# Kernel optimization log

Hardware: AMD Instinct MI355X
Metric: run time of the kernel (lower is better)

Reference implementation:

```python
import jax, jax.numpy as jnp
import numpy as np

N, IN_DIM, E_RAW, N_GRAPHS, HEADS = 50000, 128, 800000, 256, 2
NEG_ATT, NEG_ACT, EPS = 0.2, 0.01, 1e-5


def _gat(x, src, dst, W, a_src, a_dst, bias):
    # PyG GATConv: x' = xW per head; alpha = softmax_over_dst(leaky_relu(a_s.h_src + a_d.h_dst, 0.2))
    H, C = a_src.shape
    n = x.shape[0]
    h = (x @ W).reshape(n, H, C)                                  # [N,H,C]
    al_s = jnp.einsum('nhc,hc->nh', h, a_src)                     # [N,H]
    al_d = jnp.einsum('nhc,hc->nh', h, a_dst)                     # [N,H]
    e = jax.nn.leaky_relu(al_s[src] + al_d[dst], NEG_ATT)         # [E,H]
    m = jax.ops.segment_max(e, dst, num_segments=n)               # per-dst max (stable softmax)
    ee = jnp.exp(e - m[dst])
    s = jax.ops.segment_sum(ee, dst, num_segments=n)
    alpha = ee / (s[dst] + 1e-16)                                 # [E,H]
    out = jax.ops.segment_sum(h[src] * alpha[:, :, None], dst, num_segments=n)
    return out.reshape(n, H * C) + bias


def _bn(x, g, b):
    # training-mode BatchNorm1d over nodes (biased variance), eps=1e-5
    m = jnp.mean(x, 0)
    v = jnp.var(x, 0)
    return (x - m) * jax.lax.rsqrt(v + EPS) * g + b


def setup_inputs() -> dict:
    key = jax.random.key(0)
    ks = jax.random.split(key, 20)
    H, C1, C2, C3 = HEADS, 32, 64, 128
    rn = lambda i, sh, s=0.05: jax.random.normal(ks[i], sh, jnp.float32) * s
    inp = dict(
        x=jax.random.normal(ks[0], (N, IN_DIM), jnp.float32),
        edge_index=jax.random.randint(ks[1], (2, E_RAW), 0, N, jnp.int32),
        edge_weigth=jax.random.uniform(ks[2], (E_RAW,), jnp.float32),
        batch=jnp.sort(jax.random.randint(ks[3], (N,), 0, N_GRAPHS, jnp.int32)),
        W1=rn(4, (IN_DIM, H * C1)), a_src1=rn(5, (H, C1)), a_dst1=rn(6, (H, C1)),
        b1=jnp.zeros((H * C1,), jnp.float32), g1=jnp.ones((H * C1,), jnp.float32), be1=jnp.zeros((H * C1,), jnp.float32),
        W2=rn(7, (H * C1, H * C2)), a_src2=rn(8, (H, C2)), a_dst2=rn(9, (H, C2)),
        b2=jnp.zeros((H * C2,), jnp.float32), g2=jnp.ones((H * C2,), jnp.float32), be2=jnp.zeros((H * C2,), jnp.float32),
        W3=rn(10, (H * C2, H * C3)), a_src3=rn(11, (H, C3)), a_dst3=rn(12, (H, C3)),
        b3=jnp.zeros((H * C3,), jnp.float32), g3=jnp.ones((H * C3,), jnp.float32), be3=jnp.zeros((H * C3,), jnp.float32),
        Wc1=rn(13, (H * C1 + H * C2 + H * C3, 128)), bc1=jnp.zeros((128,), jnp.float32),
        Wc2=rn(14, (128, 64)), bc2=jnp.zeros((64,), jnp.float32),
        Wc3=rn(15, (64, 2)), bc3=jnp.zeros((2,), jnp.float32),
    )
    return inp


def reference(x, edge_index, edge_weigth, batch,
              W1, a_src1, a_dst1, b1, g1, be1,
              W2, a_src2, a_dst2, b2, g2, be2,
              W3, a_src3, a_dst3, b3, g3, be3,
              Wc1, bc1, Wc2, bc2, Wc3, bc3):
    n = x.shape[0]
    loops = jnp.arange(n, dtype=edge_index.dtype)  # GATConv add_self_loops=True
    src = jnp.concatenate([edge_index[0], loops])
    dst = jnp.concatenate([edge_index[1], loops])
    lr = lambda t: jax.nn.leaky_relu(t, NEG_ACT)
    x1 = lr(_bn(_gat(x, src, dst, W1, a_src1, a_dst1, b1), g1, be1))
    x2 = lr(_bn(_gat(x1, src, dst, W2, a_src2, a_dst2, b2), g2, be2))
    x3 = lr(_bn(_gat(x2, src, dst, W3, a_src3, a_dst3, b3), g3, be3))
    p = jnp.concatenate([
        jax.ops.segment_sum(x1, batch, num_segments=N_GRAPHS),
        jax.ops.segment_sum(x2, batch, num_segments=N_GRAPHS),
        jax.ops.segment_sum(x3, batch, num_segments=N_GRAPHS)], axis=1)
    h = lr(p @ Wc1 + bc1)
    h = lr(h @ Wc2 + bc2)
    return h @ Wc3 + bc3
```

## Files before the change

### kernel.cpp

```cpp
#include <hip/hip_runtime.h>
#include <hip/hip_fp16.h>
#include <math.h>

#define N_NODES 50000
#define E_RAW_N 800000
#define E_TOT   (E_RAW_N + N_NODES)
#define NGRAPH  256
#define POOL_F  448
#define SCAN_B  196
#define NSLICE  4
#define MBLK    391
#define EBLK    3321
#define PBLK    391

using f16x8 = __attribute__((ext_vector_type(8))) _Float16;
using f32x4 = __attribute__((ext_vector_type(4))) float;


template<int K, int F>
__device__ void do_wt(const float* __restrict__ W, __half* __restrict__ WT, int blk) {
    int i = blk * 256 + threadIdx.x;
    if (i >= F * (K / 8)) return;
    int f = i / (K / 8);
    int kb = (i % (K / 8)) * 8;
    __half tmp[8];
#pragma unroll
    for (int j = 0; j < 8; ++j) tmp[j] = __float2half(W[(size_t)(kb + j) * F + f]);
    *reinterpret_cast<uint4*>(WT + (size_t)f * K + kb) = *reinterpret_cast<uint4*>(tmp);
}


__global__ void k_init(int* __restrict__ deg, float* __restrict__ p,
                       float* __restrict__ bn,
                       const float* __restrict__ W1, const float* __restrict__ W2,
                       const float* __restrict__ W3, __half* __restrict__ WT1,
                       __half* __restrict__ WT2, __half* __restrict__ WT3) {
    int b = blockIdx.x;
    if (b < 448) {
        int i = b * 256 + threadIdx.x;
        if (i < N_NODES) deg[i] = 0;
        if (i < NGRAPH * POOL_F) p[i] = 0.f;
        if (i < NSLICE * 512 * 3) bn[i] = 0.f;
    } else {
        int wb = b - 448;
        if (wb < 4)       do_wt<128, 64>(W1, WT1, wb);
        else if (wb < 8)  do_wt<64, 128>(W2, WT2, wb - 4);
        else              do_wt<128, 256>(W3, WT3, wb - 8);
    }
}


__device__ inline void degrank_body(int bid, const int* __restrict__ dst_raw,
                                    int* __restrict__ deg, int* __restrict__ rank) {
    int e = bid * 256 + threadIdx.x;
    if (e >= E_TOT) return;
    int d = (e < E_RAW_N) ? dst_raw[e] : (e - E_RAW_N);
    rank[e] = atomicAdd(&deg[d], 1);
}

__global__ void k_scan1(const int* __restrict__ deg, int* __restrict__ bsum) {
    __shared__ int red[256];
    int i = blockIdx.x * 256 + threadIdx.x;
    int v = (i < N_NODES) ? deg[i] : 0;
    red[threadIdx.x] = v;
    __syncthreads();
    for (int o = 128; o > 0; o >>= 1) {
        if (threadIdx.x < o) red[threadIdx.x] += red[threadIdx.x + o];
        __syncthreads();
    }
    if (threadIdx.x == 0) bsum[blockIdx.x] = red[0];
}

__global__ void k_scan3(const int* __restrict__ deg, const int* __restrict__ bsum,
                        int* __restrict__ rowstart) {
    __shared__ int pre[256];
    __shared__ int s[256];
    int tid = threadIdx.x;
    pre[tid] = (tid < (int)blockIdx.x) ? bsum[tid] : 0;
    int i = blockIdx.x * 256 + tid;
    int v = (i < N_NODES) ? deg[i] : 0;
    s[tid] = v;
    __syncthreads();
    for (int o = 128; o > 0; o >>= 1) {
        if (tid < o) pre[tid] += pre[tid + o];
        __syncthreads();
    }
    for (int o = 1; o < 256; o <<= 1) {
        int t = (tid >= o) ? s[tid - o] : 0;
        __syncthreads();
        s[tid] += t;
        __syncthreads();
    }
    if (i < N_NODES) rowstart[i] = pre[0] + s[tid] - v;
    if (i == 0) rowstart[N_NODES] = E_TOT;
}

__global__ void k_fill(const int* __restrict__ ei, const int* __restrict__ rowstart,
                       const int* __restrict__ rank, int* __restrict__ adj) {
    int e = blockIdx.x * blockDim.x + threadIdx.x;
    if (e >= E_TOT) return;
    int s, d;
    if (e < E_RAW_N) { s = ei[e]; d = ei[E_RAW_N + e]; }
    else             { s = d = e - E_RAW_N; }
    adj[rowstart[d] + rank[e]] = s;
}


template<int F>
__device__ void bnpool_body(int bid, const __half* __restrict__ x,
                            const float* __restrict__ bnP, const float* __restrict__ g,
                            const float* __restrict__ be, const int* __restrict__ batch,
                            float* __restrict__ p, int poff) {
    constexpr int F2 = F / 2;
    constexpr int NGRP = 512 / F;
    constexpr int NPB = 128;
    int f2 = threadIdx.x % F2;
    int grp = threadIdx.x / F2;
    int f = 2 * f2;
    const float invN = 1.f / (float)N_NODES;
    float sm0 = 0.f, sm1 = 0.f, sq0 = 0.f, sq1 = 0.f;
#pragma unroll
    for (int s = 0; s < NSLICE; ++s) {
        sm0 += bnP[s * 2 * F + f];     sm1 += bnP[s * 2 * F + f + 1];
        sq0 += bnP[s * 2 * F + F + f]; sq1 += bnP[s * 2 * F + F + f + 1];
    }
    float m0 = sm0 * invN, m1 = sm1 * invN;
    float v0 = sq0 * invN - m0 * m0;
    float v1 = sq1 * invN - m1 * m1;
    float sc0 = rsqrtf(v0 + 1e-5f) * g[f];
    float sc1 = rsqrtf(v1 + 1e-5f) * g[f + 1];
    float bb0 = be[f] - m0 * sc0;
    float bb1 = be[f + 1] - m1 * sc1;
    int n0 = bid * NPB;
    int nend = n0 + NPB; if (nend > N_NODES) nend = N_NODES;
    int n = n0 + grp;
    if (n >= nend) return;
    float p0 = 0.f, p1 = 0.f;
    int cg = batch[n];
    for (; n < nend; n += NGRP) {
        float2 xv = __half22float2(*reinterpret_cast<const __half2*>(x + (size_t)n * F + f));
        float y0 = xv.x * sc0 + bb0; y0 = y0 > 0.f ? y0 : 0.01f * y0;
        float y1 = xv.y * sc1 + bb1; y1 = y1 > 0.f ? y1 : 0.01f * y1;
        int bg = batch[n];
        if (bg != cg) {
            atomicAdd(&p[cg * POOL_F + poff + f], p0);
            atomicAdd(&p[cg * POOL_F + poff + f + 1], p1);
            p0 = p1 = 0.f; cg = bg;
        }
        p0 += y0; p1 += y1;
    }
    atomicAdd(&p[cg * POOL_F + poff + f], p0);
    atomicAdd(&p[cg * POOL_F + poff + f + 1], p1);
}

template<int F>
__global__ void k_bnpool(const __half* __restrict__ x, const float* __restrict__ bnP,
                         const float* __restrict__ g, const float* __restrict__ be,
                         const int* __restrict__ batch, float* __restrict__ p, int poff) {
    bnpool_body<F>(blockIdx.x, x, bnP, g, be, batch, p, poff);
}


template<int K, int F, bool BNIN, typename TIN, typename TOUT, int SIDE>
__global__ void __launch_bounds__(256) k_mfma(
        const TIN* __restrict__ x, const __half* __restrict__ WT,
        const float* __restrict__ bnP,
        const float* __restrict__ g, const float* __restrict__ be,
        const float* __restrict__ a_src, const float* __restrict__ a_dst,
        void* __restrict__ hout, float* __restrict__ al_s, float* __restrict__ al_d,
        const int* __restrict__ dst_raw, int* __restrict__ deg, int* __restrict__ rank,
        const int* __restrict__ batch, float* __restrict__ pp, int poff) {
    if constexpr (SIDE == 1) {
        if (blockIdx.x >= MBLK) { degrank_body(blockIdx.x - MBLK, dst_raw, deg, rank); return; }
    } else if constexpr (SIDE == 2) {
        if (blockIdx.x >= MBLK) {
            bnpool_body<K>(blockIdx.x - MBLK, (const __half*)x, bnP, g, be, batch, pp, poff);
            return;
        }
    }
    constexpr int NF = F / 16;
    constexpr int KS = K / 32;
    constexpr int MT = 2;
    __shared__ float scs[K], bbs[K];
    int tid = threadIdx.x;
    if constexpr (BNIN) {
        const float invN = 1.f / (float)N_NODES;
        for (int i = tid; i < K; i += 256) {
            float sm = 0.f, sq = 0.f;
#pragma unroll
            for (int s = 0; s < NSLICE; ++s) {
                sm += bnP[s * 2 * K + i];
                sq += bnP[s * 2 * K + K + i];
            }
            float mean = sm * invN;
            float var  = sq * invN - mean * mean;
            float sc = rsqrtf(var + 1e-5f) * g[i];
            scs[i] = sc;
            bbs[i] = be[i] - mean * sc;
        }
        __syncthreads();
    }
    int wave = tid >> 6, lane = tid & 63;
    int col = lane & 15;
    int kg  = lane >> 4;
    long n_base = ((long)blockIdx.x * 4 + wave) * (MT * 16);
    if (n_base >= N_NODES) return;

    bool mv[MT];
#pragma unroll
    for (int m = 0; m < MT; ++m) mv[m] = (n_base + m * 16) < N_NODES;

    f32x4 acc[MT][NF];
#pragma unroll
    for (int m = 0; m < MT; ++m)
#pragma unroll
        for (int t = 0; t < NF; ++t) acc[m][t] = (f32x4){0.f, 0.f, 0.f, 0.f};

    for (int ks = 0; ks < KS; ++ks) {
        int kb = ks * 32 + kg * 8;
        f16x8 af[MT];
#pragma unroll
        for (int m = 0; m < MT; ++m) {
            if (!mv[m]) { af[m] = (f16x8){}; continue; }
            long nrow = n_base + m * 16 + col;
            if constexpr (sizeof(TIN) == 2) {
                uint4 u = *reinterpret_cast<const uint4*>((const __half*)x + nrow * K + kb);
                if constexpr (BNIN) {
                    const __half* hp = reinterpret_cast<const __half*>(&u);
                    f16x8 a;
#pragma unroll
                    for (int j = 0; j < 8; ++j) {
                        float y = __half2float(hp[j]) * scs[kb + j] + bbs[kb + j];
                        y = y > 0.f ? y : 0.01f * y;
                        a[j] = (_Float16)y;
                    }
                    af[m] = a;
                } else {
                    af[m] = *reinterpret_cast<const f16x8*>(&u);
                }
            } else {
                const float* xp = (const float*)x + nrow * K + kb;
                float4 v0 = *reinterpret_cast<const float4*>(xp);
                float4 v1 = *reinterpret_cast<const float4*>(xp + 4);
                f16x8 a;
                a[0] = (_Float16)v0.x; a[1] = (_Float16)v0.y;
                a[2] = (_Float16)v0.z; a[3] = (_Float16)v0.w;
                a[4] = (_Float16)v1.x; a[5] = (_Float16)v1.y;
                a[6] = (_Float16)v1.z; a[7] = (_Float16)v1.w;
                af[m] = a;
            }
        }
#pragma unroll
        for (int t = 0; t < NF; ++t) {
            f16x8 bf = *reinterpret_cast<const f16x8*>(WT + (size_t)(t * 16 + col) * K + kb);
            acc[0][t] = __builtin_amdgcn_mfma_f32_16x16x32_f16(af[0], bf, acc[0][t], 0, 0, 0);
            if constexpr (MT > 1)
                acc[1][t] = __builtin_amdgcn_mfma_f32_16x16x32_f16(af[1], bf, acc[1][t], 0, 0, 0);
        }
    }

#pragma unroll
    for (int m = 0; m < MT; ++m) {
        if (!mv[m]) continue;
#pragma unroll
        for (int t = 0; t < NF; ++t) {
#pragma unroll
            for (int r = 0; r < 4; ++r) {
                long n = n_base + m * 16 + kg * 4 + r;
                float v = acc[m][t][r];
                if constexpr (sizeof(TOUT) == 1) {
                    int pk = __builtin_amdgcn_cvt_pk_fp8_f32(v, v, 0, false);
                    reinterpret_cast<unsigned char*>(hout)[n * F + t * 16 + col] =
                        (unsigned char)(pk & 0xff);
                } else {
                    reinterpret_cast<__half*>(hout)[n * F + t * 16 + col] = __float2half(v);
                }
            }
        }
#pragma unroll
        for (int r = 0; r < 4; ++r) {
            float ss0 = 0.f, sd0 = 0.f, ss1 = 0.f, sd1 = 0.f;
#pragma unroll
            for (int t = 0; t < NF; ++t) {
                float v = acc[m][t][r];
                float as = a_src[t * 16 + col];
                float ad = a_dst[t * 16 + col];
                if (t < NF / 2) { ss0 += v * as; sd0 += v * ad; }
                else            { ss1 += v * as; sd1 += v * ad; }
            }
#pragma unroll
            for (int o = 1; o < 16; o <<= 1) {
                ss0 += __shfl_xor(ss0, o); sd0 += __shfl_xor(sd0, o);
                ss1 += __shfl_xor(ss1, o); sd1 += __shfl_xor(sd1, o);
            }
            if (col == 0) {
                long n = n_base + m * 16 + kg * 4 + r;
                al_s[n * 2]     = ss0; al_s[n * 2 + 1] = ss1;
                al_d[n * 2]     = sd0; al_d[n * 2 + 1] = sd1;
            }
        }
    }
}


template<bool FP8> struct PayT;
template<> struct PayT<false> { using T = uint4; };
template<> struct PayT<true>  { using T = uint2; };

template<bool FP8>
__device__ inline void accum8(typename PayT<FP8>::T u, float ee, float acc[8]) {
    if constexpr (FP8) {
        auto f0 = __builtin_amdgcn_cvt_pk_f32_fp8(u.x, false);
        auto f1 = __builtin_amdgcn_cvt_pk_f32_fp8(u.x, true);
        auto f2 = __builtin_amdgcn_cvt_pk_f32_fp8(u.y, false);
        auto f3 = __builtin_amdgcn_cvt_pk_f32_fp8(u.y, true);
        acc[0] += ee * f0[0]; acc[1] += ee * f0[1];
        acc[2] += ee * f1[0]; acc[3] += ee * f1[1];
        acc[4] += ee * f2[0]; acc[5] += ee * f2[1];
        acc[6] += ee * f3[0]; acc[7] += ee * f3[1];
    } else {
        float2 f0 = __half22float2(*reinterpret_cast<const __half2*>(&u.x));
        float2 f1 = __half22float2(*reinterpret_cast<const __half2*>(&u.y));
        float2 f2 = __half22float2(*reinterpret_cast<const __half2*>(&u.z));
        float2 f3 = __half22float2(*reinterpret_cast<const __half2*>(&u.w));
        acc[0] += ee * f0.x; acc[1] += ee * f0.y;
        acc[2] += ee * f1.x; acc[3] += ee * f1.y;
        acc[4] += ee * f2.x; acc[5] += ee * f2.y;
        acc[6] += ee * f3.x; acc[7] += ee * f3.y;
    }
}

template<int F, int C, bool FP8>
__global__ void __launch_bounds__(256) k_gather(
        const int* __restrict__ rowstart, const int* __restrict__ adj,
        const void* __restrict__ hv, const float* __restrict__ al_s,
        const float* __restrict__ al_d, const float* __restrict__ bias,
        __half* __restrict__ xpre) {
    using LT = typename PayT<FP8>::T;
    constexpr int HPL = 8;
    constexpr int LPE = F / HPL;
    constexpr int EPI = 64 / LPE;
    constexpr int UNR = (EPI >= 8) ? 4 : (16 / EPI);
    constexpr int STEP = UNR * EPI;
    constexpr unsigned RSH = FP8 ? 8 : ((F == 64) ? 7 : 8);
    int wave = (blockIdx.x * 256 + threadIdx.x) >> 6;
    int lane = threadIdx.x & 63;
    if (wave >= N_NODES) return;
    int n = wave;
    int rs = rowstart[n], re = rowstart[n + 1];
    float2 aldv = *reinterpret_cast<const float2*>(al_d + n * 2);

    const int es = lane / LPE;
    const int fl = lane % LPE;
    const unsigned fi = fl * HPL;
    const int hd = (fi >= C) ? 1 : 0;
    const float alh = hd ? aldv.y : aldv.x;
    const char* base = (const char*)hv;
    const char* alsb = (const char*)al_s;
    const unsigned fioff = FP8 ? fi : fi * 2;

    float acc[HPL];
#pragma unroll
    for (int j = 0; j < HPL; ++j) acc[j] = 0.f;
    float seh = 0.f;

    int nsteps = (re - rs + STEP - 1) / STEP;
    unsigned sN[UNR];
#pragma unroll
    for (int u = 0; u < UNR; ++u) {
        int e = rs + u * EPI + es;
        sN[u] = (unsigned)adj[min(e, re - 1)];
    }
    for (int t = 0; t < nsteps; ++t) {
        int ibase = rs + t * STEP;
        unsigned sC[UNR];
#pragma unroll
        for (int u = 0; u < UNR; ++u) sC[u] = sN[u];
        if (t + 1 < nsteps) {
            int nb = ibase + STEP;
#pragma unroll
            for (int u = 0; u < UNR; ++u) {
                int e = nb + u * EPI + es;
                sN[u] = (unsigned)adj[min(e, re - 1)];
            }
        }
        float alsN[UNR];
        LT hvN[UNR];
#pragma unroll
        for (int u = 0; u < UNR; ++u) {
            alsN[u] = *reinterpret_cast<const float*>(alsb + ((sC[u] << 3) | (unsigned)(hd << 2)));
            hvN[u] = *reinterpret_cast<const LT*>(base + ((sC[u] << RSH) + fioff));
        }
#pragma unroll
        for (int u = 0; u < UNR; ++u) {
            bool valid = (ibase + u * EPI + es) < re;
            float v = alsN[u] + alh; v = v > 0.f ? v : 0.2f * v;
            v = fminf(v, 80.f);
            float ee = valid ? __expf(v) : 0.f;
            seh += ee;
            accum8<FP8>(hvN[u], ee, acc);
        }
    }

#pragma unroll
    for (int o = LPE; o < 64; o <<= 1) {
        seh += __shfl_xor(seh, o);
#pragma unroll
        for (int j = 0; j < HPL; ++j) acc[j] += __shfl_xor(acc[j], o);
    }

    if (es == 0) {
        float inv = 1.f / (seh + 1e-16f);
        const float* bp = bias + fi;
        __half2 o0 = __floats2half2_rn(acc[0] * inv + bp[0], acc[1] * inv + bp[1]);
        __half2 o1 = __floats2half2_rn(acc[2] * inv + bp[2], acc[3] * inv + bp[3]);
        __half2 o2 = __floats2half2_rn(acc[4] * inv + bp[4], acc[5] * inv + bp[5]);
        __half2 o3 = __floats2half2_rn(acc[6] * inv + bp[6], acc[7] * inv + bp[7]);
        uint4 u;
        u.x = *reinterpret_cast<unsigned int*>(&o0);
        u.y = *reinterpret_cast<unsigned int*>(&o1);
        u.z = *reinterpret_cast<unsigned int*>(&o2);
        u.w = *reinterpret_cast<unsigned int*>(&o3);
        *reinterpret_cast<uint4*>(xpre + (size_t)n * F + fi) = u;
    }
}


template<int F>
__global__ void __launch_bounds__(256) k_bnstats(const __half* __restrict__ x,
        float* __restrict__ bnP) {
    constexpr int SLOTS = F / 8;
    constexpr int RPI   = 256 / SLOTS;
    __shared__ float ls[256][8];
    int tid = threadIdx.x;
    int slot = tid % SLOTS;
    int r0 = tid / SLOTS;
    int slice = blockIdx.x & (NSLICE - 1);
    float s[8], q[8];
#pragma unroll
    for (int j = 0; j < 8; ++j) { s[j] = 0.f; q[j] = 0.f; }
    int stride = gridDim.x * RPI;
    for (int n = blockIdx.x * RPI + r0; n < N_NODES; n += stride) {
        uint4 u = *reinterpret_cast<const uint4*>(x + (size_t)n * F + slot * 8);
        float2 f0 = __half22float2(*reinterpret_cast<__half2*>(&u.x));
        float2 f1 = __half22float2(*reinterpret_cast<__half2*>(&u.y));
        float2 f2 = __half22float2(*reinterpret_cast<__half2*>(&u.z));
        float2 f3 = __half22float2(*reinterpret_cast<__half2*>(&u.w));
        float v[8] = {f0.x, f0.y, f1.x, f1.y, f2.x, f2.y, f3.x, f3.y};
#pragma unroll
        for (int j = 0; j < 8; ++j) { s[j] += v[j]; q[j] += v[j] * v[j]; }
    }
#pragma unroll
    for (int j = 0; j < 8; ++j) ls[tid][j] = s[j];
    __syncthreads();
    if (tid < F) {
        int sl = tid / 8, j = tid % 8;
        float t = 0.f;
        for (int r = 0; r < RPI; ++r) t += ls[r * SLOTS + sl][j];
        atomicAdd(&bnP[slice * 2 * F + tid], t);
    }
    __syncthreads();
#pragma unroll
    for (int j = 0; j < 8; ++j) ls[tid][j] = q[j];
    __syncthreads();
    if (tid < F) {
        int sl = tid / 8, j = tid % 8;
        float t = 0.f;
        for (int r = 0; r < RPI; ++r) t += ls[r * SLOTS + sl][j];
        atomicAdd(&bnP[slice * 2 * F + F + tid], t);
    }
}


__global__ void k_mlp(const float* __restrict__ p, const float* __restrict__ Wc1,
                      const float* __restrict__ bc1, const float* __restrict__ Wc2,
                      const float* __restrict__ bc2, const float* __restrict__ Wc3,
                      const float* __restrict__ bc3, float* __restrict__ out) {
    __shared__ float pr[POOL_F];
    __shared__ float h1[128];
    __shared__ float h2[64];
    int g = blockIdx.x, tid = threadIdx.x;
    for (int i = tid; i < POOL_F; i += 128) pr[i] = p[g * POOL_F + i];
    __syncthreads();
    float a = bc1[tid];
    for (int k = 0; k < POOL_F; ++k) a += pr[k] * Wc1[k * 128 + tid];
    a = a > 0.f ? a : 0.01f * a;
    h1[tid] = a;
    __syncthreads();
    if (tid < 64) {
        float b = bc2[tid];
        for (int k = 0; k < 128; ++k) b += h1[k] * Wc2[k * 64 + tid];
        b = b > 0.f ? b : 0.01f * b;
        h2[tid] = b;
    }
    __syncthreads();
    if (tid < 2) {
        float c = bc3[tid];
        for (int k = 0; k < 64; ++k) c += h2[k] * Wc3[k * 2 + tid];
        out[g * 2 + tid] = c;
    }
}


extern "C" void kernel_launch(void* const* d_in, const int* in_sizes, int n_in,
                              void* d_out, int out_size, void* d_ws, size_t ws_size,
                              hipStream_t stream) {
    const float* x    = (const float*)d_in[0];
    const int*   ei   = (const int*)d_in[1];
    const int*   batch= (const int*)d_in[3];
    const float* W1  = (const float*)d_in[4];
    const float* as1 = (const float*)d_in[5];
    const float* ad1 = (const float*)d_in[6];
    const float* b1  = (const float*)d_in[7];
    const float* g1  = (const float*)d_in[8];
    const float* be1 = (const float*)d_in[9];
    const float* W2  = (const float*)d_in[10];
    const float* as2 = (const float*)d_in[11];
    const float* ad2 = (const float*)d_in[12];
    const float* b2  = (const float*)d_in[13];
    const float* g2  = (const float*)d_in[14];
    const float* be2 = (const float*)d_in[15];
    const float* W3  = (const float*)d_in[16];
    const float* as3 = (const float*)d_in[17];
    const float* ad3 = (const float*)d_in[18];
    const float* b3  = (const float*)d_in[19];
    const float* g3  = (const float*)d_in[20];
    const float* be3 = (const float*)d_in[21];
    const float* Wc1 = (const float*)d_in[22];
    const float* bc1 = (const float*)d_in[23];
    const float* Wc2 = (const float*)d_in[24];
    const float* bc2 = (const float*)d_in[25];
    const float* Wc3 = (const float*)d_in[26];
    const float* bc3 = (const float*)d_in[27];
    float* out = (float*)d_out;

    char* wsb = (char*)d_ws;
    size_t off = 0;
    auto alloc = [&](size_t b) -> void* {
        void* pp = wsb + off;
        off += (b + 255) & ~(size_t)255;
        return pp;
    };
    int*    adj      = (int*)alloc((size_t)E_TOT * 4);
    int*    rank     = (int*)alloc((size_t)E_TOT * 4);
    int*    rowstart = (int*)alloc((size_t)(N_NODES + 1) * 4);
    int*    deg      = (int*)alloc((size_t)N_NODES * 4);
    int*    bsum     = (int*)alloc(256 * 4);
    float*  al_s     = (float*)alloc((size_t)N_NODES * 2 * 4);
    float*  al_d     = (float*)alloc((size_t)N_NODES * 2 * 4);
    float*  bn1      = (float*)alloc(NSLICE * 512 * 4);
    float*  bn2      = (float*)alloc(NSLICE * 512 * 4);
    float*  bn3      = (float*)alloc(NSLICE * 512 * 4);
    float*  p        = (float*)alloc((size_t)NGRAPH * POOL_F * 4);
    __half* WT1      = (__half*)alloc((size_t)64 * 128 * 2);
    __half* WT2      = (__half*)alloc((size_t)128 * 64 * 2);
    __half* WT3      = (__half*)alloc((size_t)256 * 128 * 2);
    __half* hbuf     = (__half*)alloc((size_t)N_NODES * 128 * 2);
    unsigned char* h8buf = (unsigned char*)alloc((size_t)N_NODES * 256);
    __half* xbuf     = (__half*)alloc((size_t)N_NODES * 256 * 2);

    k_init<<<472, 256, 0, stream>>>(deg, p, bn1, W1, W2, W3, WT1, WT2, WT3);

    int wb = (N_NODES + 3) / 4;
    const int sb = 480;

    k_mfma<128, 64, false, float, __half, 1><<<MBLK + EBLK, 256, 0, stream>>>(
        x, WT1, nullptr, nullptr, nullptr, as1, ad1, hbuf, al_s, al_d,
        ei + E_RAW_N, deg, rank, nullptr, nullptr, 0);
    k_scan1<<<SCAN_B, 256, 0, stream>>>(deg, bsum);
    k_scan3<<<SCAN_B, 256, 0, stream>>>(deg, bsum, rowstart);
    k_fill<<<EBLK, 256, 0, stream>>>(ei, rowstart, rank, adj);

    k_gather<64, 32, false><<<wb, 256, 0, stream>>>(rowstart, adj, hbuf, al_s, al_d, b1, xbuf);
    k_bnstats<64><<<sb, 256, 0, stream>>>(xbuf, bn1);

    k_mfma<64, 128, true, __half, __half, 2><<<MBLK + PBLK, 256, 0, stream>>>(
        xbuf, WT2, bn1, g1, be1, as2, ad2, hbuf, al_s, al_d,
        nullptr, nullptr, nullptr, batch, p, 0);
    k_gather<128, 64, false><<<wb, 256, 0, stream>>>(rowstart, adj, hbuf, al_s, al_d, b2, xbuf);
    k_bnstats<128><<<sb, 256, 0, stream>>>(xbuf, bn2);

    k_mfma<128, 256, true, __half, unsigned char, 2><<<MBLK + PBLK, 256, 0, stream>>>(
        xbuf, WT3, bn2, g2, be2, as3, ad3, h8buf, al_s, al_d,
        nullptr, nullptr, nullptr, batch, p, 64);
    k_gather<256, 128, true><<<wb, 256, 0, stream>>>(rowstart, adj, h8buf, al_s, al_d, b3, xbuf);
    k_bnstats<256><<<sb, 256, 0, stream>>>(xbuf, bn3);

    k_bnpool<256><<<PBLK, 256, 0, stream>>>(xbuf, bn3, g3, be3, batch, p, 192);
    k_mlp<<<NGRAPH, 128, 0, stream>>>(p, Wc1, bc1, Wc2, bc2, Wc3, bc3, out);
}
```

Before: 291.2 us.

## Split MFMA GEMM across heads via grid y and vectorize transposed output stores

```diff
diff --git a/kernel.cpp b/kernel.cpp
--- a/kernel.cpp
+++ b/kernel.cpp
@@ -161,7 +161,7 @@
 }
 
 
-template<int K, int F, bool BNIN, typename TIN, typename TOUT, int SIDE>
+template<int K, int F, bool BNIN, bool SPLIT, typename TIN, typename TOUT, int SIDE>
 __global__ void __launch_bounds__(256) k_mfma(
         const TIN* __restrict__ x, const __half* __restrict__ WT,
         const float* __restrict__ bnP,
@@ -174,13 +174,18 @@
         if (blockIdx.x >= MBLK) { degrank_body(blockIdx.x - MBLK, dst_raw, deg, rank); return; }
     } else if constexpr (SIDE == 2) {
         if (blockIdx.x >= MBLK) {
-            bnpool_body<K>(blockIdx.x - MBLK, (const __half*)x, bnP, g, be, batch, pp, poff);
+            if (blockIdx.y == 0)
+                bnpool_body<K>(blockIdx.x - MBLK, (const __half*)x, bnP, g, be, batch, pp, poff);
             return;
         }
     }
-    constexpr int NF = F / 16;
+    constexpr int FH = SPLIT ? F / 2 : F;
+    constexpr int NF = FH / 16;
     constexpr int KS = K / 32;
     constexpr int MT = 2;
+    constexpr int C  = F / 2;
+    const int hd  = SPLIT ? (int)blockIdx.y : 0;
+    const int fof = hd * C;
     __shared__ float scs[K], bbs[K];
     int tid = threadIdx.x;
     if constexpr (BNIN) {
@@ -206,10 +211,6 @@
     long n_base = ((long)blockIdx.x * 4 + wave) * (MT * 16);
     if (n_base >= N_NODES) return;
 
-    bool mv[MT];
-#pragma unroll
-    for (int m = 0; m < MT; ++m) mv[m] = (n_base + m * 16) < N_NODES;
-
     f32x4 acc[MT][NF];
 #pragma unroll
     for (int m = 0; m < MT; ++m)
@@ -221,8 +222,8 @@
         f16x8 af[MT];
 #pragma unroll
         for (int m = 0; m < MT; ++m) {
-            if (!mv[m]) { af[m] = (f16x8){}; continue; }
             long nrow = n_base + m * 16 + col;
+            if (nrow >= N_NODES) nrow = N_NODES - 1;
             if constexpr (sizeof(TIN) == 2) {
                 uint4 u = *reinterpret_cast<const uint4*>((const __half*)x + nrow * K + kb);
                 if constexpr (BNIN) {
@@ -252,51 +253,72 @@
         }
 #pragma unroll
         for (int t = 0; t < NF; ++t) {
-            f16x8 bf = *reinterpret_cast<const f16x8*>(WT + (size_t)(t * 16 + col) * K + kb);
-            acc[0][t] = __builtin_amdgcn_mfma_f32_16x16x32_f16(af[0], bf, acc[0][t], 0, 0, 0);
+            f16x8 bf = *reinterpret_cast<const f16x8*>(WT + (size_t)(fof + t * 16 + col) * K + kb);
+            acc[0][t] = __builtin_amdgcn_mfma_f32_16x16x32_f16(bf, af[0], acc[0][t], 0, 0, 0);
             if constexpr (MT > 1)
-                acc[1][t] = __builtin_amdgcn_mfma_f32_16x16x32_f16(af[1], bf, acc[1][t], 0, 0, 0);
+                acc[1][t] = __builtin_amdgcn_mfma_f32_16x16x32_f16(bf, af[1], acc[1][t], 0, 0, 0);
         }
     }
 
 #pragma unroll
     for (int m = 0; m < MT; ++m) {
-        if (!mv[m]) continue;
+        int node_i = (int)(n_base + m * 16 + col);
+        bool ok = node_i < N_NODES;
 #pragma unroll
         for (int t = 0; t < NF; ++t) {
-#pragma unroll
-            for (int r = 0; r < 4; ++r) {
-                long n = n_base + m * 16 + kg * 4 + r;
-                float v = acc[m][t][r];
+            int fb = fof + t * 16 + kg * 4;
+            if (ok) {
                 if constexpr (sizeof(TOUT) == 1) {
-                    int pk = __builtin_amdgcn_cvt_pk_fp8_f32(v, v, 0, false);
-                    reinterpret_cast<unsigned char*>(hout)[n * F + t * 16 + col] =
-                        (unsigned char)(pk & 0xff);
+                    int pk0 = __builtin_amdgcn_cvt_pk_fp8_f32(acc[m][t][0], acc[m][t][1], 0, false);
+                    int pk1 = __builtin_amdgcn_cvt_pk_fp8_f32(acc[m][t][2], acc[m][t][3], 0, false);
+                    unsigned u = ((unsigned)pk0 & 0xffffu) | ((unsigned)pk1 << 16);
+                    *reinterpret_cast<unsigned*>((unsigned char*)hout + (size_t)node_i * F + fb) = u;
                 } else {
-                    reinterpret_cast<__half*>(hout)[n * F + t * 16 + col] = __float2half(v);
+                    __half2 p0 = __floats2half2_rn(acc[m][t][0], acc[m][t][1]);
+                    __half2 p1 = __floats2half2_rn(acc[m][t][2], acc[m][t][3]);
+                    uint2 u;
+                    u.x = *reinterpret_cast<unsigned int*>(&p0);
+                    u.y = *reinterpret_cast<unsigned int*>(&p1);
+                    *reinterpret_cast<uint2*>((__half*)hout + (size_t)node_i * F + fb) = u;
                 }
             }
         }
-#pragma unroll
-        for (int r = 0; r < 4; ++r) {
+        if constexpr (SPLIT) {
+            float ss = 0.f, sd = 0.f;
+#pragma unroll
+            for (int t = 0; t < NF; ++t) {
+#pragma unroll
+                for (int r = 0; r < 4; ++r) {
+                    int f = fof + t * 16 + kg * 4 + r;
+                    ss += acc[m][t][r] * a_src[f];
+                    sd += acc[m][t][r] * a_dst[f];
+                }
+            }
+            ss += __shfl_xor(ss, 16); ss += __shfl_xor(ss, 32);
+            sd += __shfl_xor(sd, 16); sd += __shfl_xor(sd, 32);
+            if (kg == 0 && ok) {
+                al_s[node_i * 2 + hd] = ss;
+                al_d[node_i * 2 + hd] = sd;
+            }
+        } else {
             float ss0 = 0.f, sd0 = 0.f, ss1 = 0.f, sd1 = 0.f;
 #pragma unroll
             for (int t = 0; t < NF; ++t) {
-                float v = acc[m][t][r];
-                float as = a_src[t * 16 + col];
-                float ad = a_dst[t * 16 + col];
-                if (t < NF / 2) { ss0 += v * as; sd0 += v * ad; }
-                else            { ss1 += v * as; sd1 += v * ad; }
-            }
-#pragma unroll
-            for (int o = 1; o < 16; o <<= 1) {
-                ss0 += __shfl_xor(ss0, o); sd0 += __shfl_xor(sd0, o);
-                ss1 += __shfl_xor(ss1, o); sd1 += __shfl_xor(sd1, o);
-            }
-            if (col == 0) {
-                long n = n_base + m * 16 + kg * 4 + r;
-                al_s[n * 2]     = ss0; al_s[n * 2 + 1] = ss1;
-                al_d[n * 2]     = sd0; al_d[n * 2 + 1] = sd1;
+#pragma unroll
+                for (int r = 0; r < 4; ++r) {
+                    int f = t * 16 + kg * 4 + r;
+                    float v = acc[m][t][r];
+                    if (t < NF / 2) { ss0 += v * a_src[f]; sd0 += v * a_dst[f]; }
+                    else            { ss1 += v * a_src[f]; sd1 += v * a_dst[f]; }
+                }
+            }
+            ss0 += __shfl_xor(ss0, 16); ss0 += __shfl_xor(ss0, 32);
+            sd0 += __shfl_xor(sd0, 16); sd0 += __shfl_xor(sd0, 32);
+            ss1 += __shfl_xor(ss1, 16); ss1 += __shfl_xor(ss1, 32);
+            sd1 += __shfl_xor(sd1, 16); sd1 += __shfl_xor(sd1, 32);
+            if (kg == 0 && ok) {
+                al_s[node_i * 2]     = ss0; al_s[node_i * 2 + 1] = ss1;
+                al_d[node_i * 2]     = sd0; al_d[node_i * 2 + 1] = sd1;
             }
         }
     }
@@ -564,7 +586,7 @@
     int wb = (N_NODES + 3) / 4;
     const int sb = 480;
 
-    k_mfma<128, 64, false, float, __half, 1><<<MBLK + EBLK, 256, 0, stream>>>(
+    k_mfma<128, 64, false, false, float, __half, 1><<<MBLK + EBLK, 256, 0, stream>>>(
         x, WT1, nullptr, nullptr, nullptr, as1, ad1, hbuf, al_s, al_d,
         ei + E_RAW_N, deg, rank, nullptr, nullptr, 0);
     k_scan1<<<SCAN_B, 256, 0, stream>>>(deg, bsum);
@@ -574,13 +596,13 @@
     k_gather<64, 32, false><<<wb, 256, 0, stream>>>(rowstart, adj, hbuf, al_s, al_d, b1, xbuf);
     k_bnstats<64><<<sb, 256, 0, stream>>>(xbuf, bn1);
 
-    k_mfma<64, 128, true, __half, __half, 2><<<MBLK + PBLK, 256, 0, stream>>>(
+    k_mfma<64, 128, true, true, __half, __half, 2><<<dim3(MBLK + PBLK, 2), 256, 0, stream>>>(
         xbuf, WT2, bn1, g1, be1, as2, ad2, hbuf, al_s, al_d,
         nullptr, nullptr, nullptr, batch, p, 0);
     k_gather<128, 64, false><<<wb, 256, 0, stream>>>(rowstart, adj, hbuf, al_s, al_d, b2, xbuf);
     k_bnstats<128><<<sb, 256, 0, stream>>>(xbuf, bn2);
 
-    k_mfma<128, 256, true, __half, unsigned char, 2><<<MBLK + PBLK, 256, 0, stream>>>(
+    k_mfma<128, 256, true, true, __half, unsigned char, 2><<<dim3(MBLK + PBLK, 2), 256, 0, stream>>>(
         xbuf, WT3, bn2, g2, be2, as3, ad3, h8buf, al_s, al_d,
         nullptr, nullptr, nullptr, batch, p, 64);
     k_gather<256, 128, true><<<wb, 256, 0, stream>>>(rowstart, adj, h8buf, al_s, al_d, b3, xbuf);
```

Measured after the change: 276.8 us. 1.05x faster.
